# Kernel tuning notes

Measured on AMD Instinct MI355X. Metric: run time of the kernel, lower is better.

## Reference

```python
import jax, jax.numpy as jnp
import numpy as np

S, B, I, H = 512, 64, 512, 1024  # seq_len, batch, input_size, hidden_size


def setup_inputs() -> dict:
    key = jax.random.key(0)
    k0, k1, k2, k3, k4 = jax.random.split(key, 5)
    x = jax.random.normal(k0, (S, B, I), dtype=jnp.float32)
    # nn.Linear-style init scale
    Ww = jax.random.uniform(k1, (H, H), jnp.float32, -1.0, 1.0) / np.float32(np.sqrt(H))
    Wb = jax.random.uniform(k2, (H,), jnp.float32, -1.0, 1.0) / np.float32(np.sqrt(H))
    Vw = jax.random.uniform(k3, (H, I), jnp.float32, -1.0, 1.0) / np.float32(np.sqrt(I))
    Vb = jax.random.uniform(k4, (H,), jnp.float32, -1.0, 1.0) / np.float32(np.sqrt(I))
    return {"x": x, "Ww": Ww, "Wb": Wb, "Vw": Vw, "Vb": Vb}


def reference(x, Ww, Wb, Vw, Vb):
    # h_t = tanh(W h_{t-1} + b_W + V x_t + b_V); h_0 = 0
    # Input projection has no temporal dependence -> one big batched matmul.
    Vx = jnp.einsum('sbi,hi->sbh', x, Vw) + Vb  # (S, B, H)

    def step(h, vx_t):
        h = jnp.tanh(h @ Ww.T + Wb + vx_t)
        return h, h

    h0 = jnp.zeros((x.shape[1], Ww.shape[0]), dtype=x.dtype)
    h_final, h_seq = jax.lax.scan(step, h0, Vx)
    # torch code cats the (1,B,H)-broadcast hidden states along dim 0 -> (S,B,H),
    # and returns the final hidden as (1,B,H).
    return h_seq, h_final[None]
```

## Files before the change

### kernel.cpp

```cpp
#include <hip/hip_runtime.h>
#include <math.h>

#define RS 512
#define RB 64
#define RI 512
#define RH 1024

#define NG   8
#define WPG  32
#define BPG  8

__global__ __launch_bounds__(256) void vx_gemm(const float* __restrict__ A,
                                               const float* __restrict__ W,
                                               const float* __restrict__ bias,
                                               float* __restrict__ C,
                                               int M, int N, int K) {
    __shared__ __align__(16) float As[16][68];
    __shared__ __align__(16) float Bs[16][68];

    const int tx = threadIdx.x;
    const int ty = threadIdx.y;
    const int tid = ty * 16 + tx;
    const int m0 = blockIdx.y * 64;
    const int n0 = blockIdx.x * 64;

    float acc[4][4] = {};

    const int row  = tid >> 2;
    const int quad = tid & 3;

    for (int k0 = 0; k0 < K; k0 += 16) {
        float4 av = *(const float4*)&A[(size_t)(m0 + row) * K + k0 + quad * 4];
        float4 wv = *(const float4*)&W[(size_t)(n0 + row) * K + k0 + quad * 4];
        const int kq = quad * 4;
        As[kq + 0][row] = av.x; As[kq + 1][row] = av.y;
        As[kq + 2][row] = av.z; As[kq + 3][row] = av.w;
        Bs[kq + 0][row] = wv.x; Bs[kq + 1][row] = wv.y;
        Bs[kq + 2][row] = wv.z; Bs[kq + 3][row] = wv.w;
        __syncthreads();

        #pragma unroll
        for (int k = 0; k < 16; ++k) {
            float4 a = *(const float4*)&As[k][ty * 4];
            float4 b = *(const float4*)&Bs[k][tx * 4];
            float am[4] = {a.x, a.y, a.z, a.w};
            float bn[4] = {b.x, b.y, b.z, b.w};
            #pragma unroll
            for (int i = 0; i < 4; ++i)
                #pragma unroll
                for (int j = 0; j < 4; ++j)
                    acc[i][j] = fmaf(am[i], bn[j], acc[i][j]);
        }
        __syncthreads();
    }

    #pragma unroll
    for (int i = 0; i < 4; ++i) {
        const int m = m0 + ty * 4 + i;
        const int n = n0 + tx * 4;
        float4 o;
        o.x = acc[i][0] + bias[n + 0];
        o.y = acc[i][1] + bias[n + 1];
        o.z = acc[i][2] + bias[n + 2];
        o.w = acc[i][3] + bias[n + 3];
        *(float4*)&C[(size_t)m * N + n] = o;
    }
}

__global__ __launch_bounds__(256, 1) void rnn_persistent(
    const float* __restrict__ Ww, const float* __restrict__ Wb,
    float* __restrict__ hseq, float* __restrict__ hfin,
    float* __restrict__ hex, int* __restrict__ flags)
{
    const int tid  = threadIdx.x;
    const int wgid = blockIdx.x;
    const int g    = wgid & 7;
    const int sub  = wgid >> 3;
    const int j0   = sub * 32;
    const int b0   = g * BPG;

    const int wave = tid >> 6, lane = tid & 63;
    const int kc = wave * 4 + (lane >> 4);
    const int jp = lane & 15;

    const int o_jl = tid & 31, o_bl = tid >> 5;
    const int oj = j0 + o_jl;

    float wreg[2][64];
    {
        const float* base = Ww + (size_t)(j0 + jp * 2) * RH + kc * 64;
        #pragma unroll
        for (int jj = 0; jj < 2; ++jj)
            #pragma unroll
            for (int ki = 0; ki < 64; ki += 4) {
                float4 v = *(const float4*)(base + (size_t)jj * RH + ki);
                wreg[jj][ki + 0] = v.x; wreg[jj][ki + 1] = v.y;
                wreg[jj][ki + 2] = v.z; wreg[jj][ki + 3] = v.w;
            }
    }
    const float wb = Wb[oj];

    __shared__ __align__(16) float Hs[8256];
    __shared__ __align__(16) float Red[4096];

    int* gflags = flags + g * WPG;

    for (int t = 0; t < RS; ++t) {
        float acc[16];
        #pragma unroll
        for (int i = 0; i < 16; ++i) acc[i] = 0.f;

        if (t > 0) {
            const unsigned long long* src = (const unsigned long long*)
                (hex + ((size_t)((t - 1) & 1) * NG + g) * (RH * BPG));
            #pragma unroll
            for (int i = 0; i < 16; ++i) {
                const int idx = tid + 256 * i;
                unsigned long long u = __hip_atomic_load(src + idx,
                    __ATOMIC_RELAXED, __HIP_MEMORY_SCOPE_AGENT);
                union { unsigned long long u; float f[2]; } cv; cv.u = u;
                const int k = idx >> 2, q = idx & 3;
                const int base = k * 8 + (k >> 6) * 4 + q * 2;
                Hs[base] = cv.f[0]; Hs[base + 1] = cv.f[1];
            }
            __syncthreads();

            const float4* hv = (const float4*)Hs;
            const int hbase = kc * 129;
            #pragma unroll
            for (int ki = 0; ki < 64; ++ki) {
                const float4 h0 = hv[hbase + ki * 2];
                const float4 h1 = hv[hbase + ki * 2 + 1];
                const float w0 = wreg[0][ki], w1 = wreg[1][ki];
                acc[0]  = fmaf(w0, h0.x, acc[0]);  acc[1]  = fmaf(w0, h0.y, acc[1]);
                acc[2]  = fmaf(w0, h0.z, acc[2]);  acc[3]  = fmaf(w0, h0.w, acc[3]);
                acc[4]  = fmaf(w0, h1.x, acc[4]);  acc[5]  = fmaf(w0, h1.y, acc[5]);
                acc[6]  = fmaf(w0, h1.z, acc[6]);  acc[7]  = fmaf(w0, h1.w, acc[7]);
                acc[8]  = fmaf(w1, h0.x, acc[8]);  acc[9]  = fmaf(w1, h0.y, acc[9]);
                acc[10] = fmaf(w1, h0.z, acc[10]); acc[11] = fmaf(w1, h0.w, acc[11]);
                acc[12] = fmaf(w1, h1.x, acc[12]); acc[13] = fmaf(w1, h1.y, acc[13]);
                acc[14] = fmaf(w1, h1.z, acc[14]); acc[15] = fmaf(w1, h1.w, acc[15]);
            }

            float4* rp = (float4*)&Red[(kc * 16 + jp) * 16];
            rp[0] = make_float4(acc[0],  acc[1],  acc[2],  acc[3]);
            rp[1] = make_float4(acc[4],  acc[5],  acc[6],  acc[7]);
            rp[2] = make_float4(acc[8],  acc[9],  acc[10], acc[11]);
            rp[3] = make_float4(acc[12], acc[13], acc[14], acc[15]);
            __syncthreads();
        }

        float z = 0.f;
        if (t > 0) {
            const int rbase = (o_jl >> 1) * 16 + (o_jl & 1) * 8 + o_bl;
            #pragma unroll
            for (int kk = 0; kk < 16; ++kk)
                z += Red[kk * 256 + rbase];
        }
        float* cell = hseq + (size_t)t * (RB * RH) + (size_t)(b0 + o_bl) * RH + oj;
        const float h = tanhf(z + wb + *cell);
        *cell = h;

        if (t == RS - 1) {
            hfin[(size_t)(b0 + o_bl) * RH + oj] = h;
        } else {
            __hip_atomic_store(
                hex + ((size_t)(t & 1) * NG + g) * (RH * BPG) + (size_t)oj * BPG + o_bl,
                h, __ATOMIC_RELAXED, __HIP_MEMORY_SCOPE_AGENT);
            __syncthreads();
            if (tid == 0)
                __hip_atomic_store(&gflags[sub], t + 1,
                                   __ATOMIC_RELEASE, __HIP_MEMORY_SCOPE_AGENT);
            if (wave == 0) {
                const int target = t + 1;
                const int idx = lane & 31;
                while (__hip_atomic_load(&gflags[idx], __ATOMIC_RELAXED,
                                         __HIP_MEMORY_SCOPE_AGENT) < target) {}
            }
            __syncthreads();
        }
    }
}

extern "C" void kernel_launch(void* const* d_in, const int* in_sizes, int n_in,
                              void* d_out, int out_size, void* d_ws, size_t ws_size,
                              hipStream_t stream) {
    const float* x  = (const float*)d_in[0];
    const float* Ww = (const float*)d_in[1];
    const float* Wb = (const float*)d_in[2];
    const float* Vw = (const float*)d_in[3];
    const float* Vb = (const float*)d_in[4];

    float* out  = (float*)d_out;
    float* hseq = out;
    float* hfin = out + (size_t)RS * RB * RH;

    int*   flags = (int*)d_ws;
    float* hex   = (float*)((char*)d_ws + 1024);

    {
        dim3 grid(RH / 64, (RS * RB) / 64);
        dim3 block(16, 16);
        vx_gemm<<<grid, block, 0, stream>>>(x, Vw, Vb, hseq, RS * RB, RH, RI);
    }

    rnn_persistent<<<dim3(NG * WPG), dim3(256), 0, stream>>>(Ww, Wb, hseq, hfin,
                                                             hex, flags);
}
```

Before: 7.851 ms.

## Replace block-wide step barrier with per-wave flags and wave-private hidden staging

Each wave now publishes its own sequence flag and spins on only the 32 producer flags it needs, using a wave-wide vote. This removes the two workgroup barriers and the single-thread flag store from every timestep. The hidden-state exchange layout is changed so each wave loads its slice into a private shared-memory region. The reduction buffer is double-buffered and swizzled to cut bank conflicts, the input projection is loaded early, and outputs use nontemporal stores. The looser ordering depends on per-wave release/acquire being correct across the double-buffered exchange, which is risky.

After: 10.40 ms. +32.5%, slower.

```diff
diff --git a/kernel.cpp b/kernel.cpp
--- a/kernel.cpp
+++ b/kernel.cpp
@@ -70,18 +70,19 @@
 __global__ __launch_bounds__(256, 1) void rnn_persistent(
     const float* __restrict__ Ww, const float* __restrict__ Wb,
     float* __restrict__ hseq, float* __restrict__ hfin,
-    float* __restrict__ hex, int* __restrict__ flags)
+    float* __restrict__ hex, int* __restrict__ seq)
 {
-    const int tid  = threadIdx.x;
-    const int wgid = blockIdx.x;
-    const int g    = wgid & 7;
-    const int sub  = wgid >> 3;
-    const int j0   = sub * 32;
-    const int b0   = g * BPG;
-
-    const int wave = tid >> 6, lane = tid & 63;
-    const int kc = wave * 4 + (lane >> 4);
-    const int jp = lane & 15;
+    const int tid = threadIdx.x;
+    const int g   = blockIdx.x & 7;
+    const int sub = blockIdx.x >> 3;
+    const int j0  = sub * 32;
+    const int b0  = g * BPG;
+
+    const int w    = tid >> 6;
+    const int lane = tid & 63;
+    const int kc   = w * 4 + (lane >> 4);
+    const int kc_l = lane >> 4;
+    const int jp   = lane & 15;
 
     const int o_jl = tid & 31, o_bl = tid >> 5;
     const int oj = j0 + o_jl;
@@ -100,37 +101,50 @@
     }
     const float wb = Wb[oj];
 
-    __shared__ __align__(16) float Hs[8256];
-    __shared__ __align__(16) float Red[4096];
-
-    int* gflags = flags + g * WPG;
+    __shared__ __align__(16) float Hs[4 * 2080];
+    __shared__ __align__(16) float Red[2 * 4096];
 
     for (int t = 0; t < RS; ++t) {
-        float acc[16];
-        #pragma unroll
-        for (int i = 0; i < 16; ++i) acc[i] = 0.f;
+        float* cell = hseq + (size_t)t * (RB * RH) + (size_t)(b0 + o_bl) * RH + oj;
+        const float vx = *cell;
 
         if (t > 0) {
+            const int* sq = seq + g * 128 + w * 32;
+            int v;
+            do {
+                v = 0x7fffffff;
+                if (lane < 32)
+                    v = __hip_atomic_load(sq + lane, __ATOMIC_RELAXED,
+                                          __HIP_MEMORY_SCOPE_AGENT);
+            } while (!__all(v >= t));
+
             const unsigned long long* src = (const unsigned long long*)
-                (hex + ((size_t)((t - 1) & 1) * NG + g) * (RH * BPG));
-            #pragma unroll
-            for (int i = 0; i < 16; ++i) {
-                const int idx = tid + 256 * i;
-                unsigned long long u = __hip_atomic_load(src + idx,
-                    __ATOMIC_RELAXED, __HIP_MEMORY_SCOPE_AGENT);
-                union { unsigned long long u; float f[2]; } cv; cv.u = u;
-                const int k = idx >> 2, q = idx & 3;
-                const int base = k * 8 + (k >> 6) * 4 + q * 2;
-                Hs[base] = cv.f[0]; Hs[base + 1] = cv.f[1];
-            }
-            __syncthreads();
-
-            const float4* hv = (const float4*)Hs;
-            const int hbase = kc * 129;
+                (hex + (((size_t)((t - 1) & 1)) * NG + g) * 8192)
+                + (size_t)w * 1024 + lane * 2;
+            unsigned long long dlo[8], dhi[8];
+            #pragma unroll
+            for (int c = 0; c < 8; ++c) {
+                dlo[c] = __hip_atomic_load(src + c * 128,     __ATOMIC_RELAXED,
+                                           __HIP_MEMORY_SCOPE_AGENT);
+                dhi[c] = __hip_atomic_load(src + c * 128 + 1, __ATOMIC_RELAXED,
+                                           __HIP_MEMORY_SCOPE_AGENT);
+            }
+            float* wbase = &Hs[w * 2080];
+            #pragma unroll
+            for (int c = 0; c < 8; ++c) {
+                union { unsigned long long u[2]; float4 f; } cv;
+                cv.u[0] = dlo[c]; cv.u[1] = dhi[c];
+                *(float4*)&wbase[(c >> 1) * 516 + (c & 1) * 256 + lane * 4] = cv.f;
+            }
+
+            float acc[16];
+            #pragma unroll
+            for (int i = 0; i < 16; ++i) acc[i] = 0.f;
+            const float4* hv = (const float4*)&Hs[w * 2080 + kc_l * 516];
             #pragma unroll
             for (int ki = 0; ki < 64; ++ki) {
-                const float4 h0 = hv[hbase + ki * 2];
-                const float4 h1 = hv[hbase + ki * 2 + 1];
+                const float4 h0 = hv[ki * 2];
+                const float4 h1 = hv[ki * 2 + 1];
                 const float w0 = wreg[0][ki], w1 = wreg[1][ki];
                 acc[0]  = fmaf(w0, h0.x, acc[0]);  acc[1]  = fmaf(w0, h0.y, acc[1]);
                 acc[2]  = fmaf(w0, h0.z, acc[2]);  acc[3]  = fmaf(w0, h0.w, acc[3]);
@@ -142,42 +156,36 @@
                 acc[14] = fmaf(w1, h1.z, acc[14]); acc[15] = fmaf(w1, h1.w, acc[15]);
             }
 
-            float4* rp = (float4*)&Red[(kc * 16 + jp) * 16];
-            rp[0] = make_float4(acc[0],  acc[1],  acc[2],  acc[3]);
-            rp[1] = make_float4(acc[4],  acc[5],  acc[6],  acc[7]);
-            rp[2] = make_float4(acc[8],  acc[9],  acc[10], acc[11]);
-            rp[3] = make_float4(acc[12], acc[13], acc[14], acc[15]);
+            float* rp = &Red[(t & 1) * 4096 + (kc * 16 + jp) * 16];
+            const int rot = (jp >> 1) + ((kc & 1) << 3);
+            #pragma unroll
+            for (int v2 = 0; v2 < 16; ++v2)
+                rp[(v2 + rot) & 15] = acc[v2];
             __syncthreads();
         }
 
         float z = 0.f;
         if (t > 0) {
-            const int rbase = (o_jl >> 1) * 16 + (o_jl & 1) * 8 + o_bl;
+            const int vidx = (o_jl & 1) * 8 + o_bl;
+            const int rbse = (t & 1) * 4096;
+            const int jrow = o_jl >> 1;
             #pragma unroll
             for (int kk = 0; kk < 16; ++kk)
-                z += Red[kk * 256 + rbase];
-        }
-        float* cell = hseq + (size_t)t * (RB * RH) + (size_t)(b0 + o_bl) * RH + oj;
-        const float h = tanhf(z + wb + *cell);
-        *cell = h;
+                z += Red[rbse + (kk * 16 + jrow) * 16 +
+                         ((vidx + (o_jl >> 2) + ((kk & 1) << 3)) & 15)];
+        }
+        const float h = tanhf(z + wb + vx);
+        __builtin_nontemporal_store(h, cell);
 
         if (t == RS - 1) {
             hfin[(size_t)(b0 + o_bl) * RH + oj] = h;
         } else {
             __hip_atomic_store(
-                hex + ((size_t)(t & 1) * NG + g) * (RH * BPG) + (size_t)oj * BPG + o_bl,
+                hex + (((size_t)(t & 1)) * NG + g) * 8192 + sub * 256 + o_jl * 8 + o_bl,
                 h, __ATOMIC_RELAXED, __HIP_MEMORY_SCOPE_AGENT);
-            __syncthreads();
-            if (tid == 0)
-                __hip_atomic_store(&gflags[sub], t + 1,
+            if (lane == 0)
+                __hip_atomic_store(seq + g * 128 + sub * 4 + w, t + 1,
                                    __ATOMIC_RELEASE, __HIP_MEMORY_SCOPE_AGENT);
-            if (wave == 0) {
-                const int target = t + 1;
-                const int idx = lane & 31;
-                while (__hip_atomic_load(&gflags[idx], __ATOMIC_RELAXED,
-                                         __HIP_MEMORY_SCOPE_AGENT) < target) {}
-            }
-            __syncthreads();
         }
     }
 }
@@ -195,8 +203,8 @@
     float* hseq = out;
     float* hfin = out + (size_t)RS * RB * RH;
 
-    int*   flags = (int*)d_ws;
-    float* hex   = (float*)((char*)d_ws + 1024);
+    int*   seq = (int*)d_ws;
+    float* hex = (float*)((char*)d_ws + 8192);
 
     {
         dim3 grid(RH / 64, (RS * RB) / 64);
@@ -205,5 +213,5 @@
     }
 
     rnn_persistent<<<dim3(NG * WPG), dim3(256), 0, stream>>>(Ww, Wb, hseq, hfin,
-                                                             hex, flags);
+                                                             hex, seq);
 }
```
